# Performance work log

Measured on AMD Instinct MI355X. Metric: run time of the kernel, lower is better.

## Reference

```python
import jax, jax.numpy as jnp
import numpy as np

N, E, D_IN, D, D_OUT, L = 50000, 800000, 128, 256, 64, 3
TAU0 = 0.5
LN_EPS = 1e-5


def setup_inputs() -> dict:
    key = jax.random.key(0)
    ks = jax.random.split(key, 16)
    u01 = jax.random.uniform(ks[2], (L, 2, N, 2), minval=1e-6, maxval=1.0 - 1e-6)
    gumbel = -jnp.log(-jnp.log(u01))  # standard Gumbel(0,1) noise, one draw per layer per action net
    s = lambda k, shape, fan: jax.random.normal(k, shape) * np.float32(1.0 / np.sqrt(fan))
    return {
        'x': jax.random.normal(ks[0], (N, D_IN), dtype=jnp.float32),
        'edge_index': jax.random.randint(ks[1], (2, E), 0, N),
        'gumbel_noise': gumbel,
        'W_enc': s(ks[3], (D_IN, D), D_IN), 'b_enc': jnp.zeros((D,), jnp.float32),
        'W_root': s(ks[4], (L, D, D), D), 'W_agg': s(ks[5], (L, D, D), D), 'b_env': jnp.zeros((L, D), jnp.float32),
        'Wa_in_r': s(ks[6], (D, 2), D), 'Wa_in_a': s(ks[7], (D, 2), D), 'b_in': jnp.zeros((2,), jnp.float32),
        'Wa_out_r': s(ks[8], (D, 2), D), 'Wa_out_a': s(ks[9], (D, 2), D), 'b_out': jnp.zeros((2,), jnp.float32),
        'Wt_r': s(ks[10], (D, 1), D), 'Wt_a': s(ks[11], (D, 1), D), 'b_t': jnp.zeros((1,), jnp.float32),
        'ln_g': jnp.ones((D,), jnp.float32), 'ln_b': jnp.zeros((D,), jnp.float32),
        'W_dec': s(ks[12], (D, D_OUT), D), 'b_dec': jnp.zeros((D_OUT,), jnp.float32),
    }


def reference(x, edge_index, gumbel_noise, W_enc, b_enc, W_root, W_agg, b_env,
              Wa_in_r, Wa_in_a, b_in, Wa_out_r, Wa_out_a, b_out,
              Wt_r, Wt_a, b_t, ln_g, ln_b, W_dec, b_dec):
    n = x.shape[0]
    u, v = edge_index[0], edge_index[1]  # message flows v -> u (aggregate at u)

    def conv(h, Wr, Wa, b, ew=None):
        # GraphConv-style: root transform + sum-aggregated (optionally edge-weighted) neighbor transform
        msg = h[v] if ew is None else ew[:, None] * h[v]  # [E, D]
        agg = jax.ops.segment_sum(msg, u, num_segments=n)  # [N, D]
        return h @ Wr + agg @ Wa + b

    def layernorm(h):
        m = jnp.mean(h, axis=-1, keepdims=True)
        var = jnp.mean((h - m) ** 2, axis=-1, keepdims=True)
        return (h - m) * jax.lax.rsqrt(var + LN_EPS) * ln_g + ln_b

    def gumbel_hard(logits, g, temp):
        # hard gumbel-softmax with straight-through estimator, per-node temperature
        y = jax.nn.softmax((logits + g) / temp, axis=-1)
        hard = jax.nn.one_hot(jnp.argmax(y, axis=-1), 2, dtype=y.dtype)
        return hard + y - jax.lax.stop_gradient(y)

    # env encoder + (dropout=identity) + relu
    h = jax.nn.relu(x @ W_enc + b_enc)

    for l in range(W_root.shape[0]):
        h = layernorm(h)
        in_logits = conv(h, Wa_in_r, Wa_in_a, b_in)    # [N, 2]
        out_logits = conv(h, Wa_out_r, Wa_out_a, b_out)  # [N, 2]
        t = conv(h, Wt_r, Wt_a, b_t)                   # [N, 1]
        temp = 1.0 / (jax.nn.softplus(t) + TAU0)       # TempSoftPlus: per-node inverse temperature
        in_prob = gumbel_hard(in_logits, gumbel_noise[l, 0], temp)
        out_prob = gumbel_hard(out_logits, gumbel_noise[l, 1], temp)
        ew = in_prob[:, 0][u] * out_prob[:, 0][v]      # [E] gated edge weights
        h = jax.nn.relu(conv(h, W_root[l], W_agg[l], b_env[l], ew))

    h = layernorm(h)
    return h @ W_dec + b_dec
```

## Files before the change

kernel.cpp:

```cpp
#include <hip/hip_runtime.h>
#include <cstdint>

#define NN 50000
#define EE 800000
#define DIN 128
#define DD 256
#define DOUT 64
#define NLAYERS 3
#define LN_EPS 1e-5f
#define NB_SCAN ((NN + 255) / 256)

typedef __attribute__((ext_vector_type(8))) _Float16 h8;
typedef __attribute__((ext_vector_type(4))) float f4;

__device__ __forceinline__ float waveSum(float v) {
#pragma unroll
  for (int m = 1; m < 64; m <<= 1) v += __shfl_xor(v, m, 64);
  return v;
}

__device__ __forceinline__ void splith(const float4& a, const float4& b, h8& p1, h8& p2) {
  float t[8] = {a.x, a.y, a.z, a.w, b.x, b.y, b.z, b.w};
#pragma unroll
  for (int i = 0; i < 8; ++i) {
    _Float16 x = (_Float16)t[i];
    p1[i] = x;
    p2[i] = (_Float16)(t[i] - (float)x);
  }
}

__global__ __launch_bounds__(256) void k_ln_scalars(
    const float* __restrict__ h, const float* __restrict__ ln_g, const float* __restrict__ ln_b,
    const float* __restrict__ Wir, const float* __restrict__ Wia,
    const float* __restrict__ Wor, const float* __restrict__ Woa,
    float* __restrict__ hn, float* __restrict__ SR, float* __restrict__ SA) {
  const int lane = threadIdx.x & 63;
  const int node = blockIdx.x * 4 + (threadIdx.x >> 6);
  if (node >= NN) return;
  const float4 hv = *(const float4*)(h + (size_t)node * DD + lane * 4);
  float m = waveSum(hv.x + hv.y + hv.z + hv.w) * (1.f / DD);
  float dx = hv.x - m, dy = hv.y - m, dz = hv.z - m, dw = hv.w - m;
  float var = waveSum(dx * dx + dy * dy + dz * dz + dw * dw) * (1.f / DD);
  float rs = 1.f / sqrtf(var + LN_EPS);
  const float4 g = *(const float4*)(ln_g + lane * 4);
  const float4 bb = *(const float4*)(ln_b + lane * 4);
  float4 o;
  o.x = fmaf(dx * rs, g.x, bb.x);
  o.y = fmaf(dy * rs, g.y, bb.y);
  o.z = fmaf(dz * rs, g.z, bb.z);
  o.w = fmaf(dw * rs, g.w, bb.w);
  *(float4*)(hn + (size_t)node * DD + lane * 4) = o;
  float p[8];
  const float4 a0 = *(const float4*)(Wir + 8 * lane);
  const float4 a1 = *(const float4*)(Wir + 8 * lane + 4);
  p[0] = o.x * a0.x + o.y * a0.z + o.z * a1.x + o.w * a1.z;
  p[1] = o.x * a0.y + o.y * a0.w + o.z * a1.y + o.w * a1.w;
  const float4 c0 = *(const float4*)(Wia + 8 * lane);
  const float4 c1 = *(const float4*)(Wia + 8 * lane + 4);
  p[2] = o.x * c0.x + o.y * c0.z + o.z * c1.x + o.w * c1.z;
  p[3] = o.x * c0.y + o.y * c0.w + o.z * c1.y + o.w * c1.w;
  const float4 e0 = *(const float4*)(Wor + 8 * lane);
  const float4 e1 = *(const float4*)(Wor + 8 * lane + 4);
  p[4] = o.x * e0.x + o.y * e0.z + o.z * e1.x + o.w * e1.z;
  p[5] = o.x * e0.y + o.y * e0.w + o.z * e1.y + o.w * e1.w;
  const float4 f0 = *(const float4*)(Woa + 8 * lane);
  const float4 f1 = *(const float4*)(Woa + 8 * lane + 4);
  p[6] = o.x * f0.x + o.y * f0.z + o.z * f1.x + o.w * f1.z;
  p[7] = o.x * f0.y + o.y * f0.w + o.z * f1.y + o.w * f1.w;
#pragma unroll
  for (int j = 0; j < 8; ++j) p[j] = waveSum(p[j]);
  if (lane == 0) {
    *(float4*)(SR + (size_t)node * 4) = make_float4(p[0], p[1], p[4], p[5]);
    *(float4*)(SA + (size_t)node * 4) = make_float4(p[2], p[3], p[6], p[7]);
  }
}

__global__ void k_zero_deg(int* __restrict__ deg) {
  int i = blockIdx.x * 256 + threadIdx.x;
  if (i < NN) deg[i] = 0;
}

__global__ void k_deg(const int* __restrict__ ei, int* __restrict__ deg) {
  int e = blockIdx.x * 256 + threadIdx.x;
  if (e < EE) atomicAdd(&deg[ei[e]], 1);
}

__global__ __launch_bounds__(256) void k_scan1(const int* __restrict__ deg,
                                               int* __restrict__ bsum) {
  __shared__ int sm[256];
  const int t = threadIdx.x;
  int i = blockIdx.x * 256 + t;
  sm[t] = (i < NN) ? deg[i] : 0;
  __syncthreads();
  for (int off = 128; off > 0; off >>= 1) {
    if (t < off) sm[t] += sm[t + off];
    __syncthreads();
  }
  if (t == 0) bsum[blockIdx.x] = sm[0];
}

__global__ __launch_bounds__(256) void k_scan2(const int* __restrict__ bsum,
                                               int* __restrict__ boff,
                                               int* __restrict__ rowptr) {
  __shared__ int sm[256];
  const int t = threadIdx.x;
  int v = (t < NB_SCAN) ? bsum[t] : 0;
  sm[t] = v;
  __syncthreads();
  for (int off = 1; off < 256; off <<= 1) {
    int x = (t >= off) ? sm[t - off] : 0;
    __syncthreads();
    sm[t] += x;
    __syncthreads();
  }
  if (t < NB_SCAN) boff[t] = sm[t] - v;
  if (t == 0) rowptr[NN] = sm[255];
}

__global__ __launch_bounds__(256) void k_scan3(const int* __restrict__ deg,
                                               const int* __restrict__ boff,
                                               int* __restrict__ rowptr,
                                               int* __restrict__ cursor) {
  __shared__ int sm[256];
  const int t = threadIdx.x;
  int i = blockIdx.x * 256 + t;
  int v = (i < NN) ? deg[i] : 0;
  sm[t] = v;
  __syncthreads();
  for (int off = 1; off < 256; off <<= 1) {
    int x = (t >= off) ? sm[t - off] : 0;
    __syncthreads();
    sm[t] += x;
    __syncthreads();
  }
  if (i < NN) {
    int r = boff[blockIdx.x] + sm[t] - v;
    rowptr[i] = r;
    cursor[i] = r;
  }
}

__global__ void k_fill(const int* __restrict__ ei, int* __restrict__ cursor,
                       int* __restrict__ csr_v) {
  int e = blockIdx.x * 256 + threadIdx.x;
  if (e >= EE) return;
  int u = ei[e], v = ei[EE + e];
  int slot = atomicAdd(&cursor[u], 1);
  csr_v[slot] = v;
}

__global__ void k_prep_generic(const float* __restrict__ W, int K, int N,
                               _Float16* __restrict__ W1, _Float16* __restrict__ W2) {
  int idx = blockIdx.x * 256 + threadIdx.x;
  if (idx >= K * N) return;
  int n = idx / K, k = idx - n * K;
  float w = W[(size_t)k * N + n];
  _Float16 x = (_Float16)w;
  W1[idx] = x;
  W2[idx] = (_Float16)(w - (float)x);
}

__global__ void k_prep_conv(const float* __restrict__ Wr, const float* __restrict__ Wa, int l,
                            _Float16* __restrict__ W1, _Float16* __restrict__ W2) {
  int idx = blockIdx.x * 256 + threadIdx.x;
  if (idx >= DD * 2 * DD) return;
  int n = idx >> 9, k = idx & 511;
  float w = (k < DD) ? Wr[((size_t)l * DD + k) * DD + n]
                     : Wa[((size_t)l * DD + (k - DD)) * DD + n];
  _Float16 x = (_Float16)w;
  W1[idx] = x;
  W2[idx] = (_Float16)(w - (float)x);
}

__global__ __launch_bounds__(256) void k_gates_csr(
    const int* __restrict__ rowptr, const int* __restrict__ csr_v,
    const float* __restrict__ SR, const float* __restrict__ SA,
    const float* __restrict__ gn, const float* __restrict__ b_in,
    const float* __restrict__ b_out, unsigned char* __restrict__ gin,
    unsigned char* __restrict__ gout, int l) {
  int u = blockIdx.x * 256 + threadIdx.x;
  if (u >= NN) return;
  int beg = rowptr[u], end = rowptr[u + 1];
  float4 a = make_float4(0.f, 0.f, 0.f, 0.f);
  for (int j = beg; j < end; ++j) {
    int v = csr_v[j];
    float4 s = *(const float4*)(SA + (size_t)v * 4);
    a.x += s.x; a.y += s.y; a.z += s.z; a.w += s.w;
  }
  float4 r = *(const float4*)(SR + (size_t)u * 4);
  const float* gi = gn + ((size_t)(l * 2 + 0) * NN + u) * 2;
  const float* go = gn + ((size_t)(l * 2 + 1) * NN + u) * 2;
  float li0 = r.x + a.x + b_in[0] + gi[0];
  float li1 = r.y + a.y + b_in[1] + gi[1];
  gin[u] = (li0 >= li1) ? 1 : 0;
  float lo0 = r.z + a.z + b_out[0] + go[0];
  float lo1 = r.w + a.w + b_out[1] + go[1];
  gout[u] = (lo0 >= lo1) ? 1 : 0;
}

__global__ __launch_bounds__(256) void k_wagg_csr(
    const int* __restrict__ rowptr, const int* __restrict__ csr_v,
    const unsigned char* __restrict__ gin, const unsigned char* __restrict__ gout,
    const float* __restrict__ hn, float* __restrict__ agg) {
  const int lane = threadIdx.x & 63;
  const int u = blockIdx.x * 4 + (threadIdx.x >> 6);
  if (u >= NN) return;
  float4 acc = make_float4(0.f, 0.f, 0.f, 0.f);
  float4 acc2 = make_float4(0.f, 0.f, 0.f, 0.f);
  if (gin[u]) {
    int beg = rowptr[u], end = rowptr[u + 1];
    for (int j0 = beg; j0 < end; j0 += 64) {
      int rem = end - j0;
      int v = -1;
      if (lane < rem) v = csr_v[j0 + lane];
      int ok = (v >= 0) ? (int)gout[v] : 0;
      unsigned long long mask = __ballot(ok);
      while (mask) {
        int l0 = __builtin_ctzll(mask);
        mask &= mask - 1;
        int vv0 = __shfl(v, l0);
        const float4* p0 = (const float4*)(hn + (size_t)vv0 * DD + lane * 4);
        if (mask) {
          int l1 = __builtin_ctzll(mask);
          mask &= mask - 1;
          int vv1 = __shfl(v, l1);
          const float4* p1 = (const float4*)(hn + (size_t)vv1 * DD + lane * 4);
          float4 h0 = *p0;
          float4 h1 = *p1;
          acc.x += h0.x; acc.y += h0.y; acc.z += h0.z; acc.w += h0.w;
          acc2.x += h1.x; acc2.y += h1.y; acc2.z += h1.z; acc2.w += h1.w;
        } else {
          float4 h0 = *p0;
          acc.x += h0.x; acc.y += h0.y; acc.z += h0.z; acc.w += h0.w;
        }
      }
    }
    acc.x += acc2.x; acc.y += acc2.y; acc.z += acc2.z; acc.w += acc2.w;
  }
  *(float4*)(agg + (size_t)u * DD + lane * 4) = acc;
}

#define BM 128
#define LDP 40

template <int KTOT, int ASTR, int NFN, int OSTR, bool RELU, bool DUAL>
__global__ __launch_bounds__(256, 4) void k_mfma_gemm(
    const float* __restrict__ A0, const float* __restrict__ A1,
    const _Float16* __restrict__ B1, const _Float16* __restrict__ B2,
    const float* __restrict__ bias, float* __restrict__ outp) {
  constexpr int BN = NFN * 32;
  constexpr int KSTEPS = KTOT / 32;
  __shared__ _Float16 lA1[BM * LDP], lA2[BM * LDP];
  __shared__ _Float16 lB1[BN * LDP], lB2[BN * LDP];
  const int tid = threadIdx.x;
  const int j0 = blockIdx.x * BN;
  const int i0 = blockIdx.y * BM;
  const int lane = tid & 63, w = tid >> 6;
  const int wr = w >> 1, wc = w & 1;
  const int fr = lane & 15, fs = (lane >> 4) * 8;
  const int asr = tid >> 1, asc = (tid & 1) * 16;
  int ga = i0 + asr;
  if (ga >= NN) ga = NN - 1;
  const int bsr = (BN == 128) ? (tid >> 1) : (tid >> 2);
  const int bsc = (BN == 128) ? ((tid & 1) * 16) : ((tid & 3) * 8);
  const size_t boff = (size_t)(j0 + bsr) * KTOT + bsc;

  f4 acc[4][NFN];
#pragma unroll
  for (int i = 0; i < 4; ++i)
#pragma unroll
    for (int j = 0; j < NFN; ++j) acc[i][j] = (f4){0.f, 0.f, 0.f, 0.f};

  float4 fa0, fa1, fa2, fa3;
  h8 rb1a, rb1b, rb2a, rb2b;
  {
    const float* pa;
    if constexpr (DUAL) pa = A0 + (size_t)ga * DD + asc;
    else pa = A0 + (size_t)ga * ASTR + asc;
    fa0 = *(const float4*)(pa);     fa1 = *(const float4*)(pa + 4);
    fa2 = *(const float4*)(pa + 8); fa3 = *(const float4*)(pa + 12);
    rb1a = *(const h8*)(B1 + boff);
    rb2a = *(const h8*)(B2 + boff);
    if constexpr (BN == 128) {
      rb1b = *(const h8*)(B1 + boff + 8);
      rb2b = *(const h8*)(B2 + boff + 8);
    }
  }
  for (int kt = 0; kt < KSTEPS; ++kt) {
    __syncthreads();
    {
      int o = asr * LDP + asc;
      h8 p1a, p1b, p2a, p2b;
      splith(fa0, fa1, p1a, p2a);
      splith(fa2, fa3, p1b, p2b);
      *(h8*)&lA1[o] = p1a; *(h8*)&lA1[o + 8] = p1b;
      *(h8*)&lA2[o] = p2a; *(h8*)&lA2[o + 8] = p2b;
      int ob = bsr * LDP + bsc;
      *(h8*)&lB1[ob] = rb1a;
      *(h8*)&lB2[ob] = rb2a;
      if constexpr (BN == 128) {
        *(h8*)&lB1[ob + 8] = rb1b;
        *(h8*)&lB2[ob + 8] = rb2b;
      }
    }
    __syncthreads();
    if (kt < KSTEPS - 1) {
      int kb = (kt + 1) * 32;
      const float* pa;
      if constexpr (DUAL) {
        const float* ab = (kb < DD) ? A0 : A1;
        pa = ab + (size_t)ga * DD + (kb & (DD - 1)) + asc;
      } else {
        pa = A0 + (size_t)ga * ASTR + kb + asc;
      }
      fa0 = *(const float4*)(pa);     fa1 = *(const float4*)(pa + 4);
      fa2 = *(const float4*)(pa + 8); fa3 = *(const float4*)(pa + 12);
      rb1a = *(const h8*)(B1 + boff + kb);
      rb2a = *(const h8*)(B2 + boff + kb);
      if constexpr (BN == 128) {
        rb1b = *(const h8*)(B1 + boff + kb + 8);
        rb2b = *(const h8*)(B2 + boff + kb + 8);
      }
    }
    h8 a1[4], a2[4];
#pragma unroll
    for (int mi = 0; mi < 4; ++mi) {
      int r = (wr * 64 + mi * 16 + fr) * LDP + fs;
      a1[mi] = *(const h8*)&lA1[r];
      a2[mi] = *(const h8*)&lA2[r];
    }
#pragma unroll
    for (int ni = 0; ni < NFN; ++ni) {
      int c = (wc * (NFN * 16) + ni * 16 + fr) * LDP + fs;
      h8 b1 = *(const h8*)&lB1[c];
      h8 b2 = *(const h8*)&lB2[c];
#pragma unroll
      for (int mi = 0; mi < 4; ++mi) {
        acc[mi][ni] = __builtin_amdgcn_mfma_f32_16x16x32_f16(a1[mi], b1, acc[mi][ni], 0, 0, 0);
        acc[mi][ni] = __builtin_amdgcn_mfma_f32_16x16x32_f16(a1[mi], b2, acc[mi][ni], 0, 0, 0);
        acc[mi][ni] = __builtin_amdgcn_mfma_f32_16x16x32_f16(a2[mi], b1, acc[mi][ni], 0, 0, 0);
      }
    }
  }
#pragma unroll
  for (int ni = 0; ni < NFN; ++ni) {
    int col = j0 + wc * (NFN * 16) + ni * 16 + fr;
    float bv = bias[col];
#pragma unroll
    for (int mi = 0; mi < 4; ++mi) {
      int rbase = i0 + wr * 64 + mi * 16 + (lane >> 4) * 4;
#pragma unroll
      for (int r = 0; r < 4; ++r) {
        int row = rbase + r;
        if (row < NN) {
          float v = acc[mi][ni][r] + bv;
          outp[(size_t)row * OSTR + col] = RELU ? fmaxf(v, 0.f) : v;
        }
      }
    }
  }
}

extern "C" void kernel_launch(void* const* d_in, const int* in_sizes, int n_in,
                              void* d_out, int out_size, void* d_ws, size_t ws_size,
                              hipStream_t stream) {
  const float* x = (const float*)d_in[0];
  const int* ei = (const int*)d_in[1];
  const float* gn = (const float*)d_in[2];
  const float* W_enc = (const float*)d_in[3];
  const float* b_enc = (const float*)d_in[4];
  const float* W_root = (const float*)d_in[5];
  const float* W_agg = (const float*)d_in[6];
  const float* b_env = (const float*)d_in[7];
  const float* Wa_in_r = (const float*)d_in[8];
  const float* Wa_in_a = (const float*)d_in[9];
  const float* b_in = (const float*)d_in[10];
  const float* Wa_out_r = (const float*)d_in[11];
  const float* Wa_out_a = (const float*)d_in[12];
  const float* b_out = (const float*)d_in[13];
  const float* ln_g = (const float*)d_in[17];
  const float* ln_b = (const float*)d_in[18];
  const float* W_dec = (const float*)d_in[19];
  const float* b_dec = (const float*)d_in[20];
  float* out = (float*)d_out;

  float* ws = (float*)d_ws;
  size_t off = 0;
  float* h = ws + off;    off += (size_t)NN * DD;
  float* hn = ws + off;   off += (size_t)NN * DD;
  float* agg = ws + off;  off += (size_t)NN * DD;
  float* SR = ws + off;   off += (size_t)NN * 4;
  float* SA = ws + off;   off += (size_t)NN * 4;
  int* rowptr = (int*)(ws + off); off += (size_t)NN + 4;
  int* csr_v = (int*)(ws + off);  off += (size_t)EE;
  unsigned char* gin = (unsigned char*)(ws + off);  off += (size_t)NN / 4;
  unsigned char* gout = (unsigned char*)(ws + off); off += (size_t)NN / 4;
  _Float16* cW1 = (_Float16*)(ws + off); off += (size_t)DD * 2 * DD / 2;
  _Float16* cW2 = (_Float16*)(ws + off); off += (size_t)DD * 2 * DD / 2;
  _Float16* eW1 = (_Float16*)(ws + off); off += (size_t)DD * DIN / 2;
  _Float16* eW2 = (_Float16*)(ws + off); off += (size_t)DD * DIN / 2;
  _Float16* dW1 = (_Float16*)(ws + off); off += (size_t)DOUT * DD / 2;
  _Float16* dW2 = (_Float16*)(ws + off); off += (size_t)DOUT * DD / 2;
  if (ws_size < off * sizeof(float)) return;
  int* deg = (int*)SR;
  int* bsum = (int*)SR + NN;
  int* boff = (int*)SR + NN + 256;
  int* cursor = (int*)SA;

  k_zero_deg<<<(NN + 255) / 256, 256, 0, stream>>>(deg);
  k_deg<<<(EE + 255) / 256, 256, 0, stream>>>(ei, deg);
  k_scan1<<<NB_SCAN, 256, 0, stream>>>(deg, bsum);
  k_scan2<<<1, 256, 0, stream>>>(bsum, boff, rowptr);
  k_scan3<<<NB_SCAN, 256, 0, stream>>>(deg, boff, rowptr, cursor);
  k_fill<<<(EE + 255) / 256, 256, 0, stream>>>(ei, cursor, csr_v);

  k_prep_generic<<<(DIN * DD + 255) / 256, 256, 0, stream>>>(W_enc, DIN, DD, eW1, eW2);
  k_prep_generic<<<(DD * DOUT + 255) / 256, 256, 0, stream>>>(W_dec, DD, DOUT, dW1, dW2);

  const int gy = (NN + BM - 1) / BM;
  k_mfma_gemm<DIN, DIN, 4, DD, true, false><<<dim3(2, gy), 256, 0, stream>>>(
      x, nullptr, eW1, eW2, b_enc, h);

  for (int l = 0; l < NLAYERS; ++l) {
    k_ln_scalars<<<(NN + 3) / 4, 256, 0, stream>>>(h, ln_g, ln_b, Wa_in_r, Wa_in_a,
                                                   Wa_out_r, Wa_out_a, hn, SR, SA);
    k_gates_csr<<<(NN + 255) / 256, 256, 0, stream>>>(rowptr, csr_v, SR, SA, gn,
                                                      b_in, b_out, gin, gout, l);
    k_wagg_csr<<<(NN + 3) / 4, 256, 0, stream>>>(rowptr, csr_v, gin, gout, hn, agg);
    k_prep_conv<<<(DD * 2 * DD + 255) / 256, 256, 0, stream>>>(W_root, W_agg, l, cW1, cW2);
    k_mfma_gemm<2 * DD, DD, 4, DD, true, true><<<dim3(2, gy), 256, 0, stream>>>(
        hn, agg, cW1, cW2, b_env + (size_t)l * DD, h);
  }

  k_ln_scalars<<<(NN + 3) / 4, 256, 0, stream>>>(h, ln_g, ln_b, Wa_in_r, Wa_in_a,
                                                 Wa_out_r, Wa_out_a, hn, SR, SA);
  k_mfma_gemm<DD, DD, 2, DOUT, false, false><<<dim3(1, gy), 256, 0, stream>>>(
      hn, nullptr, dW1, dW2, b_dec, out);
}
```

Measured before the change: 737.5 us.

## Store normalized features and aggregates as pre-split fp16 pairs; shrink GEMM tile

LayerNorm output and neighbor aggregates are now stored as hi/lo fp16 pairs instead of fp32. The GEMM therefore loads ready-made fp16 operands and skips the per-tile split. Gather traffic is unchanged per row (two halves equal one float), but the split work moves out of the GEMM. The GEMM row tile drops from 128 to 64 for more blocks, and the weight-prep kernels are merged into one upfront launch each for all layers, removing per-layer prep launches. Summing hi+lo halves in the gather adds conversion ALU work, and storing aggregates as split fp16 could cost a little precision.

```diff
diff --git a/kernel.cpp b/kernel.cpp
--- a/kernel.cpp
+++ b/kernel.cpp
@@ -11,6 +11,7 @@
 #define NB_SCAN ((NN + 255) / 256)
 
 typedef __attribute__((ext_vector_type(8))) _Float16 h8;
+typedef __attribute__((ext_vector_type(4))) _Float16 h4;
 typedef __attribute__((ext_vector_type(4))) float f4;
 
 __device__ __forceinline__ float waveSum(float v) {
@@ -29,11 +30,22 @@
   }
 }
 
+__device__ __forceinline__ void split4(const float4& a, h4& q1, h4& q2) {
+  float t[4] = {a.x, a.y, a.z, a.w};
+#pragma unroll
+  for (int i = 0; i < 4; ++i) {
+    _Float16 x = (_Float16)t[i];
+    q1[i] = x;
+    q2[i] = (_Float16)(t[i] - (float)x);
+  }
+}
+
 __global__ __launch_bounds__(256) void k_ln_scalars(
     const float* __restrict__ h, const float* __restrict__ ln_g, const float* __restrict__ ln_b,
     const float* __restrict__ Wir, const float* __restrict__ Wia,
     const float* __restrict__ Wor, const float* __restrict__ Woa,
-    float* __restrict__ hn, float* __restrict__ SR, float* __restrict__ SA) {
+    _Float16* __restrict__ hn1, _Float16* __restrict__ hn2,
+    float* __restrict__ SR, float* __restrict__ SA) {
   const int lane = threadIdx.x & 63;
   const int node = blockIdx.x * 4 + (threadIdx.x >> 6);
   if (node >= NN) return;
@@ -49,7 +61,12 @@
   o.y = fmaf(dy * rs, g.y, bb.y);
   o.z = fmaf(dz * rs, g.z, bb.z);
   o.w = fmaf(dw * rs, g.w, bb.w);
-  *(float4*)(hn + (size_t)node * DD + lane * 4) = o;
+  {
+    h4 q1, q2;
+    split4(o, q1, q2);
+    *(h4*)(hn1 + (size_t)node * DD + lane * 4) = q1;
+    *(h4*)(hn2 + (size_t)node * DD + lane * 4) = q2;
+  }
   float p[8];
   const float4 a0 = *(const float4*)(Wir + 8 * lane);
   const float4 a1 = *(const float4*)(Wir + 8 * lane + 4);
@@ -149,27 +166,38 @@
   csr_v[slot] = v;
 }
 
-__global__ void k_prep_generic(const float* __restrict__ W, int K, int N,
-                               _Float16* __restrict__ W1, _Float16* __restrict__ W2) {
-  int idx = blockIdx.x * 256 + threadIdx.x;
-  if (idx >= K * N) return;
-  int n = idx / K, k = idx - n * K;
-  float w = W[(size_t)k * N + n];
-  _Float16 x = (_Float16)w;
-  W1[idx] = x;
-  W2[idx] = (_Float16)(w - (float)x);
-}
-
-__global__ void k_prep_conv(const float* __restrict__ Wr, const float* __restrict__ Wa, int l,
+__global__ void k_prep_conv(const float* __restrict__ Wr, const float* __restrict__ Wa,
                             _Float16* __restrict__ W1, _Float16* __restrict__ W2) {
   int idx = blockIdx.x * 256 + threadIdx.x;
-  if (idx >= DD * 2 * DD) return;
-  int n = idx >> 9, k = idx & 511;
+  if (idx >= NLAYERS * DD * 2 * DD) return;
+  int l = idx >> 17;
+  int rem = idx & 131071;
+  int n = rem >> 9, k = rem & 511;
   float w = (k < DD) ? Wr[((size_t)l * DD + k) * DD + n]
                      : Wa[((size_t)l * DD + (k - DD)) * DD + n];
   _Float16 x = (_Float16)w;
   W1[idx] = x;
   W2[idx] = (_Float16)(w - (float)x);
+}
+
+__global__ void k_prep_ed(const float* __restrict__ We, const float* __restrict__ Wd,
+                          _Float16* __restrict__ E1, _Float16* __restrict__ E2,
+                          _Float16* __restrict__ D1, _Float16* __restrict__ D2) {
+  int idx = blockIdx.x * 256 + threadIdx.x;
+  if (idx < DIN * DD) {
+    int n = idx / DIN, k = idx - n * DIN;
+    float w = We[(size_t)k * DD + n];
+    _Float16 x = (_Float16)w;
+    E1[idx] = x;
+    E2[idx] = (_Float16)(w - (float)x);
+  } else if (idx < DIN * DD + DD * DOUT) {
+    int j = idx - DIN * DD;
+    int n = j / DD, k = j - n * DD;
+    float w = Wd[(size_t)k * DOUT + n];
+    _Float16 x = (_Float16)w;
+    D1[j] = x;
+    D2[j] = (_Float16)(w - (float)x);
+  }
 }
 
 __global__ __launch_bounds__(256) void k_gates_csr(
@@ -201,7 +229,8 @@
 __global__ __launch_bounds__(256) void k_wagg_csr(
     const int* __restrict__ rowptr, const int* __restrict__ csr_v,
     const unsigned char* __restrict__ gin, const unsigned char* __restrict__ gout,
-    const float* __restrict__ hn, float* __restrict__ agg) {
+    const _Float16* __restrict__ hn1, const _Float16* __restrict__ hn2,
+    _Float16* __restrict__ agg1, _Float16* __restrict__ agg2) {
   const int lane = threadIdx.x & 63;
   const int u = blockIdx.x * 4 + (threadIdx.x >> 6);
   if (u >= NN) return;
@@ -219,33 +248,42 @@
         int l0 = __builtin_ctzll(mask);
         mask &= mask - 1;
         int vv0 = __shfl(v, l0);
-        const float4* p0 = (const float4*)(hn + (size_t)vv0 * DD + lane * 4);
+        const h4* p0a = (const h4*)(hn1 + (size_t)vv0 * DD + lane * 4);
+        const h4* p0b = (const h4*)(hn2 + (size_t)vv0 * DD + lane * 4);
         if (mask) {
           int l1 = __builtin_ctzll(mask);
           mask &= mask - 1;
           int vv1 = __shfl(v, l1);
-          const float4* p1 = (const float4*)(hn + (size_t)vv1 * DD + lane * 4);
-          float4 h0 = *p0;
-          float4 h1 = *p1;
-          acc.x += h0.x; acc.y += h0.y; acc.z += h0.z; acc.w += h0.w;
-          acc2.x += h1.x; acc2.y += h1.y; acc2.z += h1.z; acc2.w += h1.w;
+          const h4* p1a = (const h4*)(hn1 + (size_t)vv1 * DD + lane * 4);
+          const h4* p1b = (const h4*)(hn2 + (size_t)vv1 * DD + lane * 4);
+          h4 a0 = *p0a, b0 = *p0b, a1 = *p1a, b1 = *p1b;
+          acc.x += (float)a0[0] + (float)b0[0]; acc.y += (float)a0[1] + (float)b0[1];
+          acc.z += (float)a0[2] + (float)b0[2]; acc.w += (float)a0[3] + (float)b0[3];
+          acc2.x += (float)a1[0] + (float)b1[0]; acc2.y += (float)a1[1] + (float)b1[1];
+          acc2.z += (float)a1[2] + (float)b1[2]; acc2.w += (float)a1[3] + (float)b1[3];
         } else {
-          float4 h0 = *p0;
-          acc.x += h0.x; acc.y += h0.y; acc.z += h0.z; acc.w += h0.w;
+          h4 a0 = *p0a, b0 = *p0b;
+          acc.x += (float)a0[0] + (float)b0[0]; acc.y += (float)a0[1] + (float)b0[1];
+          acc.z += (float)a0[2] + (float)b0[2]; acc.w += (float)a0[3] + (float)b0[3];
         }
       }
     }
     acc.x += acc2.x; acc.y += acc2.y; acc.z += acc2.z; acc.w += acc2.w;
   }
-  *(float4*)(agg + (size_t)u * DD + lane * 4) = acc;
-}
-
-#define BM 128
+  h4 q1, q2;
+  split4(acc, q1, q2);
+  *(h4*)(agg1 + (size_t)u * DD + lane * 4) = q1;
+  *(h4*)(agg2 + (size_t)u * DD + lane * 4) = q2;
+}
+
+#define BM 64
 #define LDP 40
 
-template <int KTOT, int ASTR, int NFN, int OSTR, bool RELU, bool DUAL>
+template <int KTOT, int ASTR, int NFN, int OSTR, bool RELU, bool FP16A, bool DUAL>
 __global__ __launch_bounds__(256, 4) void k_mfma_gemm(
-    const float* __restrict__ A0, const float* __restrict__ A1,
+    const float* __restrict__ Af,
+    const _Float16* __restrict__ A1a, const _Float16* __restrict__ A2a,
+    const _Float16* __restrict__ A1b, const _Float16* __restrict__ A2b,
     const _Float16* __restrict__ B1, const _Float16* __restrict__ B2,
     const float* __restrict__ bias, float* __restrict__ outp) {
   constexpr int BN = NFN * 32;
@@ -258,27 +296,31 @@
   const int lane = tid & 63, w = tid >> 6;
   const int wr = w >> 1, wc = w & 1;
   const int fr = lane & 15, fs = (lane >> 4) * 8;
-  const int asr = tid >> 1, asc = (tid & 1) * 16;
+  const int asr = tid >> 2, asc = (tid & 3) * 8;
   int ga = i0 + asr;
   if (ga >= NN) ga = NN - 1;
   const int bsr = (BN == 128) ? (tid >> 1) : (tid >> 2);
   const int bsc = (BN == 128) ? ((tid & 1) * 16) : ((tid & 3) * 8);
   const size_t boff = (size_t)(j0 + bsr) * KTOT + bsc;
 
-  f4 acc[4][NFN];
-#pragma unroll
-  for (int i = 0; i < 4; ++i)
+  f4 acc[2][NFN];
+#pragma unroll
+  for (int i = 0; i < 2; ++i)
 #pragma unroll
     for (int j = 0; j < NFN; ++j) acc[i][j] = (f4){0.f, 0.f, 0.f, 0.f};
 
-  float4 fa0, fa1, fa2, fa3;
+  float4 fa0, fa1;
+  h8 ra1, ra2;
   h8 rb1a, rb1b, rb2a, rb2b;
   {
-    const float* pa;
-    if constexpr (DUAL) pa = A0 + (size_t)ga * DD + asc;
-    else pa = A0 + (size_t)ga * ASTR + asc;
-    fa0 = *(const float4*)(pa);     fa1 = *(const float4*)(pa + 4);
-    fa2 = *(const float4*)(pa + 8); fa3 = *(const float4*)(pa + 12);
+    if constexpr (FP16A) {
+      ra1 = *(const h8*)(A1a + (size_t)ga * ASTR + asc);
+      ra2 = *(const h8*)(A2a + (size_t)ga * ASTR + asc);
+    } else {
+      const float* pa = Af + (size_t)ga * ASTR + asc;
+      fa0 = *(const float4*)(pa);
+      fa1 = *(const float4*)(pa + 4);
+    }
     rb1a = *(const h8*)(B1 + boff);
     rb2a = *(const h8*)(B2 + boff);
     if constexpr (BN == 128) {
@@ -290,11 +332,15 @@
     __syncthreads();
     {
       int o = asr * LDP + asc;
-      h8 p1a, p1b, p2a, p2b;
-      splith(fa0, fa1, p1a, p2a);
-      splith(fa2, fa3, p1b, p2b);
-      *(h8*)&lA1[o] = p1a; *(h8*)&lA1[o + 8] = p1b;
-      *(h8*)&lA2[o] = p2a; *(h8*)&lA2[o + 8] = p2b;
+      if constexpr (FP16A) {
+        *(h8*)&lA1[o] = ra1;
+        *(h8*)&lA2[o] = ra2;
+      } else {
+        h8 p1, p2;
+        splith(fa0, fa1, p1, p2);
+        *(h8*)&lA1[o] = p1;
+        *(h8*)&lA2[o] = p2;
+      }
       int ob = bsr * LDP + bsc;
       *(h8*)&lB1[ob] = rb1a;
       *(h8*)&lB2[ob] = rb2a;
@@ -306,15 +352,23 @@
     __syncthreads();
     if (kt < KSTEPS - 1) {
       int kb = (kt + 1) * 32;
-      const float* pa;
-      if constexpr (DUAL) {
-        const float* ab = (kb < DD) ? A0 : A1;
-        pa = ab + (size_t)ga * DD + (kb & (DD - 1)) + asc;
+      if constexpr (FP16A) {
+        const _Float16 *s1, *s2;
+        int kk;
+        if constexpr (DUAL) {
+          s1 = (kb < DD) ? A1a : A1b;
+          s2 = (kb < DD) ? A2a : A2b;
+          kk = kb & (DD - 1);
+        } else {
+          s1 = A1a; s2 = A2a; kk = kb;
+        }
+        ra1 = *(const h8*)(s1 + (size_t)ga * ASTR + kk + asc);
+        ra2 = *(const h8*)(s2 + (size_t)ga * ASTR + kk + asc);
       } else {
-        pa = A0 + (size_t)ga * ASTR + kb + asc;
-      }
-      fa0 = *(const float4*)(pa);     fa1 = *(const float4*)(pa + 4);
-      fa2 = *(const float4*)(pa + 8); fa3 = *(const float4*)(pa + 12);
+        const float* pa = Af + (size_t)ga * ASTR + kb + asc;
+        fa0 = *(const float4*)(pa);
+        fa1 = *(const float4*)(pa + 4);
+      }
       rb1a = *(const h8*)(B1 + boff + kb);
       rb2a = *(const h8*)(B2 + boff + kb);
       if constexpr (BN == 128) {
@@ -322,10 +376,10 @@
         rb2b = *(const h8*)(B2 + boff + kb + 8);
       }
     }
-    h8 a1[4], a2[4];
-#pragma unroll
-    for (int mi = 0; mi < 4; ++mi) {
-      int r = (wr * 64 + mi * 16 + fr) * LDP + fs;
+    h8 a1[2], a2[2];
+#pragma unroll
+    for (int mi = 0; mi < 2; ++mi) {
+      int r = (wr * 32 + mi * 16 + fr) * LDP + fs;
       a1[mi] = *(const h8*)&lA1[r];
       a2[mi] = *(const h8*)&lA2[r];
     }
@@ -335,7 +389,7 @@
       h8 b1 = *(const h8*)&lB1[c];
       h8 b2 = *(const h8*)&lB2[c];
 #pragma unroll
-      for (int mi = 0; mi < 4; ++mi) {
+      for (int mi = 0; mi < 2; ++mi) {
         acc[mi][ni] = __builtin_amdgcn_mfma_f32_16x16x32_f16(a1[mi], b1, acc[mi][ni], 0, 0, 0);
         acc[mi][ni] = __builtin_amdgcn_mfma_f32_16x16x32_f16(a1[mi], b2, acc[mi][ni], 0, 0, 0);
         acc[mi][ni] = __builtin_amdgcn_mfma_f32_16x16x32_f16(a2[mi], b1, acc[mi][ni], 0, 0, 0);
@@ -347,8 +401,8 @@
     int col = j0 + wc * (NFN * 16) + ni * 16 + fr;
     float bv = bias[col];
 #pragma unroll
-    for (int mi = 0; mi < 4; ++mi) {
-      int rbase = i0 + wr * 64 + mi * 16 + (lane >> 4) * 4;
+    for (int mi = 0; mi < 2; ++mi) {
+      int rbase = i0 + wr * 32 + mi * 16 + (lane >> 4) * 4;
 #pragma unroll
       for (int r = 0; r < 4; ++r) {
         int row = rbase + r;
@@ -387,16 +441,18 @@
   float* ws = (float*)d_ws;
   size_t off = 0;
   float* h = ws + off;    off += (size_t)NN * DD;
-  float* hn = ws + off;   off += (size_t)NN * DD;
-  float* agg = ws + off;  off += (size_t)NN * DD;
+  _Float16* hn1 = (_Float16*)(ws + off);  off += (size_t)NN * DD / 2;
+  _Float16* hn2 = (_Float16*)(ws + off);  off += (size_t)NN * DD / 2;
+  _Float16* agg1 = (_Float16*)(ws + off); off += (size_t)NN * DD / 2;
+  _Float16* agg2 = (_Float16*)(ws + off); off += (size_t)NN * DD / 2;
   float* SR = ws + off;   off += (size_t)NN * 4;
   float* SA = ws + off;   off += (size_t)NN * 4;
   int* rowptr = (int*)(ws + off); off += (size_t)NN + 4;
   int* csr_v = (int*)(ws + off);  off += (size_t)EE;
   unsigned char* gin = (unsigned char*)(ws + off);  off += (size_t)NN / 4;
   unsigned char* gout = (unsigned char*)(ws + off); off += (size_t)NN / 4;
-  _Float16* cW1 = (_Float16*)(ws + off); off += (size_t)DD * 2 * DD / 2;
-  _Float16* cW2 = (_Float16*)(ws + off); off += (size_t)DD * 2 * DD / 2;
+  _Float16* cW1 = (_Float16*)(ws + off); off += (size_t)NLAYERS * DD * DD;
+  _Float16* cW2 = (_Float16*)(ws + off); off += (size_t)NLAYERS * DD * DD;
   _Float16* eW1 = (_Float16*)(ws + off); off += (size_t)DD * DIN / 2;
   _Float16* eW2 = (_Float16*)(ws + off); off += (size_t)DD * DIN / 2;
   _Float16* dW1 = (_Float16*)(ws + off); off += (size_t)DOUT * DD / 2;
@@ -404,36 +460,39 @@
   if (ws_size < off * sizeof(float)) return;
   int* deg = (int*)SR;
   int* bsum = (int*)SR + NN;
-  int* boff = (int*)SR + NN + 256;
+  int* boffp = (int*)SR + NN + 256;
   int* cursor = (int*)SA;
 
   k_zero_deg<<<(NN + 255) / 256, 256, 0, stream>>>(deg);
   k_deg<<<(EE + 255) / 256, 256, 0, stream>>>(ei, deg);
   k_scan1<<<NB_SCAN, 256, 0, stream>>>(deg, bsum);
-  k_scan2<<<1, 256, 0, stream>>>(bsum, boff, rowptr);
-  k_scan3<<<NB_SCAN, 256, 0, stream>>>(deg, boff, rowptr, cursor);
+  k_scan2<<<1, 256, 0, stream>>>(bsum, boffp, rowptr);
+  k_scan3<<<NB_SCAN, 256, 0, stream>>>(deg, boffp, rowptr, cursor);
   k_fill<<<(EE + 255) / 256, 256, 0, stream>>>(ei, cursor, csr_v);
 
-  k_prep_generic<<<(DIN * DD + 255) / 256, 256, 0, stream>>>(W_enc, DIN, DD, eW1, eW2);
-  k_prep_generic<<<(DD * DOUT + 255) / 256, 256, 0, stream>>>(W_dec, DD, DOUT, dW1, dW2);
+  k_prep_conv<<<(NLAYERS * DD * 2 * DD + 255) / 256, 256, 0, stream>>>(W_root, W_agg, cW1, cW2);
+  k_prep_ed<<<(DIN * DD + DD * DOUT + 255) / 256, 256, 0, stream>>>(W_enc, W_dec,
+                                                                    eW1, eW2, dW1, dW2);
 
   const int gy = (NN + BM - 1) / BM;
-  k_mfma_gemm<DIN, DIN, 4, DD, true, false><<<dim3(2, gy), 256, 0, stream>>>(
-      x, nullptr, eW1, eW2, b_enc, h);
+  k_mfma_gemm<DIN, DIN, 4, DD, true, false, false><<<dim3(2, gy), 256, 0, stream>>>(
+      x, nullptr, nullptr, nullptr, nullptr, eW1, eW2, b_enc, h);
 
   for (int l = 0; l < NLAYERS; ++l) {
     k_ln_scalars<<<(NN + 3) / 4, 256, 0, stream>>>(h, ln_g, ln_b, Wa_in_r, Wa_in_a,
-                                                   Wa_out_r, Wa_out_a, hn, SR, SA);
+                                                   Wa_out_r, Wa_out_a, hn1, hn2, SR, SA);
     k_gates_csr<<<(NN + 255) / 256, 256, 0, stream>>>(rowptr, csr_v, SR, SA, gn,
                                                       b_in, b_out, gin, gout, l);
-    k_wagg_csr<<<(NN + 3) / 4, 256, 0, stream>>>(rowptr, csr_v, gin, gout, hn, agg);
-    k_prep_conv<<<(DD * 2 * DD + 255) / 256, 256, 0, stream>>>(W_root, W_agg, l, cW1, cW2);
-    k_mfma_gemm<2 * DD, DD, 4, DD, true, true><<<dim3(2, gy), 256, 0, stream>>>(
-        hn, agg, cW1, cW2, b_env + (size_t)l * DD, h);
+    k_wagg_csr<<<(NN + 3) / 4, 256, 0, stream>>>(rowptr, csr_v, gin, gout,
+                                                 hn1, hn2, agg1, agg2);
+    k_mfma_gemm<2 * DD, DD, 4, DD, true, true, true><<<dim3(2, gy), 256, 0, stream>>>(
+        nullptr, hn1, hn2, agg1, agg2,
+        cW1 + (size_t)l * DD * 2 * DD, cW2 + (size_t)l * DD * 2 * DD,
+        b_env + (size_t)l * DD, h);
   }
 
   k_ln_scalars<<<(NN + 3) / 4, 256, 0, stream>>>(h, ln_g, ln_b, Wa_in_r, Wa_in_a,
-                                                 Wa_out_r, Wa_out_a, hn, SR, SA);
-  k_mfma_gemm<DD, DD, 2, DOUT, false, false><<<dim3(1, gy), 256, 0, stream>>>(
-      hn, nullptr, dW1, dW2, b_dec, out);
-}
+                                                 Wa_out_r, Wa_out_a, hn1, hn2, SR, SA);
+  k_mfma_gemm<DD, DD, 2, DOUT, false, true, false><<<dim3(1, gy), 256, 0, stream>>>(
+      nullptr, hn1, hn2, nullptr, nullptr, dW1, dW2, b_dec, out);
+}
```

After: 763.6 us. +3.5%, slower.
